# Performance work log

Hardware: AMD Instinct MI355X
Metric: run time of the kernel (lower is better)

## Reference

```python
import jax, jax.numpy as jnp
import numpy as np

DT = 1.0
S = 64            # num_sites
D = 2 * S         # state_dim
LOG_2PI = float(np.log(2.0 * np.pi))

def _selectors():
    s0 = np.zeros((2, 4), np.float32); s0[:, 0:2] = np.eye(2)
    s1 = np.zeros((2, 4), np.float32); s1[:, 2:4] = np.eye(2)
    cr = 0.5 * (s0 + s1)
    # [target=2, source=2, 2, 4]; off-diagonal pairs use the averaged selector
    return jnp.asarray(np.stack([np.stack([s0, cr]), np.stack([cr, s1])]))

SEL = _selectors()

def project_lon_lat(lon, lat):
    # lon, lat: [B,S]
    lat0 = lat.mean(-1, keepdims=True)
    lon0 = lon.mean(-1, keepdims=True)
    km = 111.32
    x = (lon - lon0) * (km * jnp.cos(jnp.deg2rad(lat0)))
    y = (lat - lat0) * km
    coords = jnp.stack([x, y], -1)                        # [B,S,2]
    h = coords[:, :, None, :] - coords[:, None, :, :]
    dist = jnp.sqrt((h ** 2).sum(-1) + 1e-12)
    npos = (dist > 1e-6).sum((-1, -2)).astype(coords.dtype)
    scale = dist.sum((-1, -2)) / jnp.maximum(npos, 1.0)
    return coords / jnp.maximum(scale, 1e-6)[:, None, None]

def build_A(h, mu, sigma, coupling, damping, eyeD):
    # h: [B,S,S,2], mu: [B,4], sigma: [B,4,4]
    B = mu.shape[0]
    sigma = 0.5 * (sigma + jnp.swapaxes(sigma, -1, -2))
    dm = jnp.einsum('tsab,nb->tsna', SEL, mu)                     # [2,2,B,2]
    dc = jnp.einsum('tsab,nbc,tsdc->tsnad', SEL, sigma, SEL)      # [2,2,B,2,2]
    dc = 0.5 * (dc + jnp.swapaxes(dc, -1, -2))
    eye2 = jnp.eye(2, dtype=h.dtype)
    Dm = (1.0 + 1e-4) * eye2 + (2.0 * DT ** 2) * dc
    Dinv = jnp.linalg.inv(Dm)
    _, logdet = jnp.linalg.slogdet(Dm)
    diff = h[None, None] - DT * dm[:, :, :, None, None, :]        # [2,2,B,S,S,2]
    q = jnp.einsum('tsbijd,tsbdf,tsbijf->tsbij', diff, Dinv, diff)
    ker = jnp.exp(-0.5 * (q + logdet[..., None, None]))
    ker = ker / jnp.maximum(ker.sum(-1, keepdims=True), 1e-6)
    ker = jnp.moveaxis(ker, 2, 0)                                 # [B,2,2,S,S]
    op = ker * coupling[None, :, :, None, None]
    op = jnp.transpose(op, (0, 1, 3, 2, 4)).reshape(B, D, D)
    return eyeD + DT * (op - damping * eyeD)

def _update(m, P, z_t, r2, eyeD):
    # Kalman measurement update with H = I, R = r2*I; returns per-sample NLL term
    Sm = P + r2 * eyeD
    v = z_t - m
    Sinv_v = jnp.linalg.solve(Sm, v[..., None])[..., 0]
    _, logdet = jnp.linalg.slogdet(Sm)
    nll_t = 0.5 * ((v * Sinv_v).sum(-1) + logdet + D * LOG_2PI)
    K = jnp.swapaxes(jnp.linalg.solve(Sm, P), -1, -2)   # P @ Sm^{-1} (P, Sm symmetric)
    m = m + jnp.einsum('bij,bj->bi', K, v)
    P = jnp.einsum('bij,bjk->bik', eyeD - K, P)
    return m, P, nll_t

def reference(z_seq, site_lon, site_lat, mu_seq, sigma_seq,
              log_q_proc, log_r_obs, log_p0, log_damping,
              init_mean, coupling_raw):
    B, T = z_seq.shape[0], z_seq.shape[1]
    z = z_seq.reshape(B, T, D)
    dtype = z.dtype
    eyeD = jnp.eye(D, dtype=dtype)
    r2 = jnp.exp(log_r_obs) ** 2
    q2 = jnp.exp(log_q_proc) ** 2
    damping = jnp.exp(log_damping)
    coupling = jnp.eye(2, dtype=dtype) + 0.25 * jnp.tanh(coupling_raw)

    lon = jnp.broadcast_to(site_lon[None], (B, S))
    lat = jnp.broadcast_to(site_lat[None], (B, S))
    coords = project_lon_lat(lon, lat)
    h = coords[:, :, None, :] - coords[:, None, :, :]   # [B,S,S,2]

    m0 = jnp.broadcast_to(init_mean[None], (B, D))
    P0 = jnp.broadcast_to(jnp.exp(log_p0) ** 2 * eyeD, (B, D, D))
    m, P, nll0 = _update(m0, P0, z[:, 0], r2, eyeD)

    def step(carry, xs):
        m, P = carry
        mu_t, sigma_t, z_t = xs
        A = build_A(h, mu_t, sigma_t, coupling, damping, eyeD)
        m = jnp.einsum('bij,bj->bi', A, m)
        P = jnp.einsum('bij,bjk,blk->bil', A, P, A) + q2 * eyeD
        m, P, nll_t = _update(m, P, z_t, r2, eyeD)
        return (m, P), nll_t

    xs = (jnp.swapaxes(mu_seq, 0, 1), jnp.swapaxes(sigma_seq, 0, 1),
          jnp.swapaxes(z[:, 1:], 0, 1))
    (_, _), nll_rest = jax.lax.scan(step, (m, P), xs)
    nll = nll0 + nll_rest.sum(0)   # [B]
    return nll.mean()

def setup_inputs() -> dict:
    key = jax.random.key(0)
    ks = jax.random.split(key, 5)
    B, T = 16, 128
    z_seq = jax.random.normal(ks[0], (B, T, S, 2), jnp.float32)
    site_lon = 10.0 + 0.5 * jax.random.uniform(ks[1], (S,), jnp.float32)
    site_lat = 55.0 + 0.5 * jax.random.uniform(ks[2], (S,), jnp.float32)
    mu_seq = 0.5 * jax.random.normal(ks[3], (B, T - 1, 4), jnp.float32)
    L = 0.2 * jax.random.normal(ks[4], (B, T - 1, 4, 4), jnp.float32)
    sigma_seq = jnp.einsum('btij,btkj->btik', L, L)   # PSD covariances
    return {
        'z_seq': z_seq, 'site_lon': site_lon, 'site_lat': site_lat,
        'mu_seq': mu_seq, 'sigma_seq': sigma_seq,
        'log_q_proc': jnp.float32(-2.0), 'log_r_obs': jnp.float32(-2.0),
        'log_p0': jnp.float32(0.0), 'log_damping': jnp.float32(0.0),
        'init_mean': jnp.zeros((D,), jnp.float32),
        'coupling_raw': jnp.zeros((2, 2), jnp.float32),
    }
```

## Files before the change

### kernel.cpp

```cpp
#include <hip/hip_runtime.h>
#include <math.h>


#define SQ 64
#define DQ 128
#define TQ 128
#define BQ 16
#define LDP 132
#define LDB 136
#define WFLOATS 17408
#define NTH 1024
#define LOG2PI 1.8378770664093454f

#define SMEM_FLOATS 35472

typedef __attribute__((ext_vector_type(8))) short bf16x8;
typedef __attribute__((ext_vector_type(4))) float f32x4;

__device__ __forceinline__ void lds_fence() {
  __asm__ volatile("s_waitcnt lgkmcnt(0)" ::: "memory");
}

__device__ __forceinline__ unsigned short f2bf(float f) {
  unsigned u = __float_as_uint(f);
  u += 0x7fffu + ((u >> 16) & 1u);
  return (unsigned short)(u >> 16);
}
__device__ __forceinline__ uint4 pack8(const float* v) {
  uint4 r;
  r.x = (unsigned)f2bf(v[0]) | ((unsigned)f2bf(v[1]) << 16);
  r.y = (unsigned)f2bf(v[2]) | ((unsigned)f2bf(v[3]) << 16);
  r.z = (unsigned)f2bf(v[4]) | ((unsigned)f2bf(v[5]) << 16);
  r.w = (unsigned)f2bf(v[6]) | ((unsigned)f2bf(v[7]) << 16);
  return r;
}

__device__ __forceinline__ float block_reduce_sum(float v, float* red) {
  #pragma unroll
  for (int off = 32; off > 0; off >>= 1) v += __shfl_down(v, off);
  const int tid = threadIdx.x;
  if ((tid & 63) == 0) red[tid >> 6] = v;
  __syncthreads();
  v = 0.0f;
  #pragma unroll
  for (int w = 0; w < NTH / 64; w++) v += red[w];
  __syncthreads();
  return v;
}

__device__ __forceinline__ void chol16_f(float* __restrict__ Wf,
                                         float* __restrict__ mdiag,
                                         int b0, int lane) {
  float a[16];
  if (lane < 16) {
    const float4* rp = (const float4*)(Wf + (b0 + lane) * LDP + b0);
    float4 q0 = rp[0], q1 = rp[1], q2v = rp[2], q3 = rp[3];
    a[0]=q0.x; a[1]=q0.y; a[2]=q0.z; a[3]=q0.w;
    a[4]=q1.x; a[5]=q1.y; a[6]=q1.z; a[7]=q1.w;
    a[8]=q2v.x; a[9]=q2v.y; a[10]=q2v.z; a[11]=q2v.w;
    a[12]=q3.x; a[13]=q3.y; a[14]=q3.z; a[15]=q3.w;
  } else {
    #pragma unroll
    for (int i = 0; i < 16; i++) a[i] = 1.0f;
  }
  float myrinv = 1.0f;
  #pragma unroll
  for (int j = 0; j < 16; j++) {
    float dj = __shfl(a[j], j);
    float rinv = rsqrtf(dj);
    float lij = a[j] * rinv;
    a[j] = lij;
    if (lane == j) myrinv = rinv;
    #pragma unroll
    for (int k = j + 1; k < 16; k++) {
      float lkj = __shfl(lij, k);
      a[k] = fmaf(-lij, lkj, a[k]);
    }
  }
  if (lane < 16) {
    float4* rp = (float4*)(Wf + (b0 + lane) * LDP + b0);
    rp[0] = make_float4(a[0], a[1], a[2], a[3]);
    rp[1] = make_float4(a[4], a[5], a[6], a[7]);
    rp[2] = make_float4(a[8], a[9], a[10], a[11]);
    rp[3] = make_float4(a[12], a[13], a[14], a[15]);
    mdiag[b0 + lane] = myrinv;
  }
}

__device__ __forceinline__ void trinv_chain2(float* __restrict__ Wf,
                                             const float* __restrict__ mdiag,
                                             int J, int pass, int lane) {
  const int c16 = lane & 15;
  const int j16 = 4 * (lane >> 4) + pass;
  const int sh = lane & 48;
  {
    float row[16];
    const float4* rp = (const float4*)(Wf + (J * 16 + c16) * LDP + J * 16);
    float4 a0 = rp[0], a1 = rp[1], a2 = rp[2], a3 = rp[3];
    row[0]=a0.x; row[1]=a0.y; row[2]=a0.z; row[3]=a0.w;
    row[4]=a1.x; row[5]=a1.y; row[6]=a1.z; row[7]=a1.w;
    row[8]=a2.x; row[9]=a2.y; row[10]=a2.z; row[11]=a2.w;
    row[12]=a3.x; row[13]=a3.y; row[14]=a3.z; row[15]=a3.w;
    float s = (c16 == j16) ? 1.0f : 0.0f;
    #pragma unroll
    for (int k = 0; k < 16; k++) {
      if (c16 == k) s *= mdiag[J * 16 + k];
      float sk = __shfl(s, sh | k);
      if (c16 > k) s = fmaf(-row[k], sk, s);
    }
    if (c16 > j16) Wf[(J * 16 + j16) * LDP + (J * 16 + c16)] = s;
  }
  lds_fence();
  const float md = mdiag[J * 16 + j16];
  const float* Mrow = Wf + (J * 16 + j16) * LDP + J * 16;
  #pragma unroll 1
  for (int I = J + 1; I < 8; I++) {
    const float* Lrow = Wf + (I * 16 + c16) * LDP + J * 16;
    float g = 0.0f;
    #pragma unroll
    for (int c4 = 0; c4 < 4; c4++) {
      float4 lv = *(const float4*)&Lrow[c4 * 4];
      float4 mq = *(const float4*)&Mrow[c4 * 4];
      float w0 = (c4*4+0 > j16) ? mq.x : ((c4*4+0 == j16) ? md : 0.0f);
      float w1 = (c4*4+1 > j16) ? mq.y : ((c4*4+1 == j16) ? md : 0.0f);
      float w2 = (c4*4+2 > j16) ? mq.z : ((c4*4+2 == j16) ? md : 0.0f);
      float w3 = (c4*4+3 > j16) ? mq.w : ((c4*4+3 == j16) ? md : 0.0f);
      g = fmaf(lv.x, w0, g); g = fmaf(lv.y, w1, g);
      g = fmaf(lv.z, w2, g); g = fmaf(lv.w, w3, g);
    }
    for (int K = J + 1; K < I; K++) {
      const float* LK = Lrow + (K - J) * 16;
      const float* MK = Wf + (J * 16 + j16) * LDP + K * 16;
      #pragma unroll
      for (int c4 = 0; c4 < 4; c4++) {
        float4 lv = *(const float4*)&LK[c4 * 4];
        float4 mq = *(const float4*)&MK[c4 * 4];
        g = fmaf(lv.x, mq.x, g); g = fmaf(lv.y, mq.y, g);
        g = fmaf(lv.z, mq.z, g); g = fmaf(lv.w, mq.w, g);
      }
    }
    float row2[16];
    {
      const float4* rp2 = (const float4*)(Wf + (I * 16 + c16) * LDP + I * 16);
      float4 a0 = rp2[0], a1 = rp2[1], a2 = rp2[2], a3 = rp2[3];
      row2[0]=a0.x; row2[1]=a0.y; row2[2]=a0.z; row2[3]=a0.w;
      row2[4]=a1.x; row2[5]=a1.y; row2[6]=a1.z; row2[7]=a1.w;
      row2[8]=a2.x; row2[9]=a2.y; row2[10]=a2.z; row2[11]=a2.w;
      row2[12]=a3.x; row2[13]=a3.y; row2[14]=a3.z; row2[15]=a3.w;
    }
    float sv = g;
    #pragma unroll
    for (int k = 0; k < 16; k++) {
      if (c16 == k) sv *= mdiag[I * 16 + k];
      float sk = __shfl(sv, sh | k);
      if (c16 > k) sv = fmaf(-row2[k], sk, sv);
    }
    Wf[(J * 16 + j16) * LDP + (I * 16 + c16)] = -sv;
    lds_fence();
  }
}

extern "C" __global__ __launch_bounds__(NTH, 4)
void ide_kf_kernel(const float* __restrict__ z_seq,
                   const float* __restrict__ site_lon,
                   const float* __restrict__ site_lat,
                   const float* __restrict__ mu_seq,
                   const float* __restrict__ sigma_seq,
                   const float* __restrict__ log_q,
                   const float* __restrict__ log_r,
                   const float* __restrict__ log_p0,
                   const float* __restrict__ log_damp,
                   const float* __restrict__ init_mean,
                   const float* __restrict__ coupling_raw,
                   float* __restrict__ ws) {
  extern __shared__ float smem[];
  float* Wf     = smem;
  float* B1f    = Wf + WFLOATS;
  float* B2f    = B1f + 8704;
  float* coords = B2f + 8704;
  float* mv     = coords + 128;
  float* vv     = mv + DQ;
  float* yv     = vv + DQ;
  float* mdiag  = yv + DQ;
  float* red    = mdiag + DQ;

  unsigned short* Tb  = (unsigned short*)Wf;
  unsigned short* Ab  = (unsigned short*)B1f;
  unsigned short* Mtb = (unsigned short*)B1f;
  unsigned short* Pb  = (unsigned short*)B2f;

  const int tid = threadIdx.x;
  const int lane = tid & 63;
  const int wave = tid >> 6;
  const int rb = wave >> 1, ch = wave & 1;
  const int m16 = lane & 15, quad = lane >> 4;
  const int grp = wave >> 2, pass = wave & 3;
  const int b = blockIdx.x;
  float* nll_out = ws;

  const float r2 = __expf(2.0f * log_r[0]);
  const float q2 = __expf(2.0f * log_q[0]);
  const float p0sq = __expf(2.0f * log_p0[0]);
  const float damping = __expf(log_damp[0]);
  const float cpl00 = 1.0f + 0.25f * tanhf(coupling_raw[0]);
  const float cpl01 = 0.25f * tanhf(coupling_raw[1]);
  const float cpl10 = 0.25f * tanhf(coupling_raw[2]);
  const float cpl11 = 1.0f + 0.25f * tanhf(coupling_raw[3]);

  float myLon = (tid < SQ) ? site_lon[tid] : 0.0f;
  float myLat = (tid < SQ) ? site_lat[tid] : 0.0f;
  float lat0 = block_reduce_sum(myLat, red) * (1.0f / 64.0f);
  float lon0 = block_reduce_sum(myLon, red) * (1.0f / 64.0f);
  if (tid < SQ) {
    const float km = 111.32f;
    float cs = cosf(lat0 * 0.017453292519943295f);
    coords[2 * tid]     = (myLon - lon0) * (km * cs);
    coords[2 * tid + 1] = (myLat - lat0) * km;
  }
  __syncthreads();
  float dsum = 0.0f, dcnt = 0.0f;
  for (int idx = tid; idx < SQ * SQ; idx += NTH) {
    int i = idx >> 6, j = idx & 63;
    float dx = coords[2 * i] - coords[2 * j];
    float dy = coords[2 * i + 1] - coords[2 * j + 1];
    float d = sqrtf(dx * dx + dy * dy + 1e-12f);
    dsum += d;
    if (d > 1e-6f) dcnt += 1.0f;
  }
  dsum = block_reduce_sum(dsum, red);
  dcnt = block_reduce_sum(dcnt, red);
  float scale = dsum / fmaxf(dcnt, 1.0f);
  float sdiv = 1.0f / fmaxf(scale, 1e-6f);
  if (tid < SQ) { coords[2 * tid] *= sdiv; coords[2 * tid + 1] *= sdiv; }

  for (int e = tid; e < WFLOATS / 4; e += NTH)
    ((float4*)Wf)[e] = make_float4(0.0f, 0.0f, 0.0f, 0.0f);
  for (int e = tid; e < 8704 / 4; e += NTH)
    ((float4*)B2f)[e] = make_float4(0.0f, 0.0f, 0.0f, 0.0f);
  __syncthreads();
  if (tid < DQ) {
    Wf[tid * LDP + tid] = p0sq + r2;
    Pb[tid * LDB + tid] = f2bf(p0sq);
    mv[tid] = init_mean[tid];
  }
  __syncthreads();

  float nllp = 0.0f;

  #pragma unroll 1
  for (int t = 0; t < TQ; t++) {
    const float* zt = z_seq + ((size_t)b * TQ + t) * DQ;

    if (t > 0) {
      const float* mu_t = mu_seq + ((size_t)b * (TQ - 1) + (t - 1)) * 4;
      const float* sg_t = sigma_seq + ((size_t)b * (TQ - 1) + (t - 1)) * 16;

      {
        const int unit = tid >> 2, q = tid & 3;
        const int r = unit >> 1, ss = unit & 1, tt = r >> 6, i = r & 63;
        float m0 = mu_t[0], m1 = mu_t[1], m2 = mu_t[2], m3 = mu_t[3];
        float dmx, dmy, c00, c01, c11;
        if (tt == 0 && ss == 0) {
          dmx = m0; dmy = m1;
          c00 = sg_t[0]; c01 = 0.5f * (sg_t[1] + sg_t[4]); c11 = sg_t[5];
        } else if (tt == 1 && ss == 1) {
          dmx = m2; dmy = m3;
          c00 = sg_t[10]; c01 = 0.5f * (sg_t[11] + sg_t[14]); c11 = sg_t[15];
        } else {
          dmx = 0.5f * (m0 + m2); dmy = 0.5f * (m1 + m3);
          float s00 = sg_t[0];
          float s02 = 0.5f * (sg_t[2] + sg_t[8]);
          float s22 = sg_t[10];
          float s01 = 0.5f * (sg_t[1] + sg_t[4]);
          float s03 = 0.5f * (sg_t[3] + sg_t[12]);
          float s21 = 0.5f * (sg_t[9] + sg_t[6]);
          float s23 = 0.5f * (sg_t[11] + sg_t[14]);
          float s11 = sg_t[5];
          float s13 = 0.5f * (sg_t[7] + sg_t[13]);
          float s33 = sg_t[15];
          c00 = 0.25f * (s00 + s02 + s02 + s22);
          c01 = 0.25f * (s01 + s03 + s21 + s23);
          c11 = 0.25f * (s11 + s13 + s13 + s33);
        }
        float D00 = 1.0001f + 2.0f * c00;
        float D01 = 2.0f * c01;
        float D11 = 1.0001f + 2.0f * c11;
        float det = D00 * D11 - D01 * D01;
        float dinv = 1.0f / det;
        float d00 = D11 * dinv, d01 = -D01 * dinv, d11 = D00 * dinv;
        float ldts = __logf(det);
        float cix = coords[2 * i], ciy = coords[2 * i + 1];
        const float* cj = coords + q * 32;
        float kv[16];
        float rsum = 0.0f;
        #pragma unroll
        for (int u = 0; u < 16; u++) {
          float dx = cix - cj[2 * u] - dmx;
          float dy = ciy - cj[2 * u + 1] - dmy;
          float qf = d00 * dx * dx + 2.0f * d01 * dx * dy + d11 * dy * dy;
          kv[u] = __expf(-0.5f * (qf + ldts));
          rsum += kv[u];
        }
        float rtot = rsum + __shfl_xor(rsum, 1);
        rtot += __shfl_xor(rtot, 2);
        float cv = (tt == 0) ? ((ss == 0) ? cpl00 : cpl01)
                             : ((ss == 0) ? cpl10 : cpl11);
        float norm = cv / fmaxf(rtot, 1e-6f);
        #pragma unroll
        for (int u = 0; u < 16; u++) kv[u] *= norm;
        if (ss == tt && ((i >> 4) == q)) kv[i & 15] += 1.0f - damping;
        unsigned short* arow = Ab + r * LDB + ss * 64 + q * 16;
        *(uint4*)(arow) = pack8(kv);
        *(uint4*)(arow + 8) = pack8(kv + 8);
      }
      __syncthreads();

      {
        f32x4 acc[4];
        #pragma unroll
        for (int c = 0; c < 4; c++) acc[c] = (f32x4){0.0f, 0.0f, 0.0f, 0.0f};
        #pragma unroll
        for (int ks = 0; ks < 4; ks++) {
          const int ko = 32 * ks + 8 * quad;
          bf16x8 a = *(const bf16x8*)(Ab + (16 * rb + m16) * LDB + ko);
          #pragma unroll
          for (int ct = 0; ct < 4; ct++) {
            bf16x8 bb = *(const bf16x8*)(Pb + (64 * ch + 16 * ct + m16) * LDB + ko);
            acc[ct] = __builtin_amdgcn_mfma_f32_16x16x32_bf16(a, bb, acc[ct], 0, 0, 0);
          }
        }
        #pragma unroll
        for (int ct = 0; ct < 4; ct++)
          #pragma unroll
          for (int reg = 0; reg < 4; reg++)
            Tb[(16 * rb + 4 * quad + reg) * LDB + 64 * ch + 16 * ct + m16] =
                f2bf(acc[ct][reg]);
        __syncthreads();
      }

      {
        const int ctmax = rb - 4 * ch;
        f32x4 acc[4];
        #pragma unroll
        for (int c = 0; c < 4; c++) acc[c] = (f32x4){0.0f, 0.0f, 0.0f, 0.0f};
        const bool gemv_wave = (wave == 1 || wave == 3);
        const int grow = (wave == 1) ? lane : 64 + lane;
        float newm = 0.0f;
        if (ctmax >= 0) {
          #pragma unroll
          for (int ks = 0; ks < 4; ks++) {
            const int ko = 32 * ks + 8 * quad;
            bf16x8 a = *(const bf16x8*)(Tb + (16 * rb + m16) * LDB + ko);
            #pragma unroll
            for (int ct = 0; ct < 4; ct++) {
              if (ct <= ctmax) {
                bf16x8 bb = *(const bf16x8*)(Ab + (64 * ch + 16 * ct + m16) * LDB + ko);
                acc[ct] = __builtin_amdgcn_mfma_f32_16x16x32_bf16(a, bb, acc[ct], 0, 0, 0);
              }
            }
          }
        } else if (gemv_wave) {
          const unsigned* ar = (const unsigned*)(Ab + grow * LDB);
          #pragma unroll 8
          for (int k2 = 0; k2 < 64; k2++) {
            unsigned p = ar[k2];
            newm = fmaf(__uint_as_float(p << 16), mv[2 * k2], newm);
            newm = fmaf(__uint_as_float(p & 0xffff0000u), mv[2 * k2 + 1], newm);
          }
        }
        __syncthreads();
        if (ctmax >= 0) {
          #pragma unroll
          for (int ct = 0; ct < 4; ct++) {
            if (ct <= ctmax) {
              #pragma unroll
              for (int reg = 0; reg < 4; reg++) {
                const int rg = 16 * rb + 4 * quad + reg;
                const int cgl = 64 * ch + 16 * ct + m16;
                Wf[rg * LDP + cgl] = acc[ct][reg] + ((rg == cgl) ? (q2 + r2) : 0.0f);
              }
            }
          }
        }
        if (gemv_wave) vv[grow] = zt[grow] - newm;
        if (wave == 0) {
          lds_fence();
          chol16_f(Wf, mdiag, 0, lane);
        }
        __syncthreads();
      }
    }

    if (t == 0) {
      if (tid < 64) {
        chol16_f(Wf, mdiag, 0, lane);
      } else if (tid < 192) {
        const int i = tid - 64;
        vv[i] = zt[i] - mv[i];
      }
      __syncthreads();
    }

    #pragma unroll 1
    for (int kb = 0; kb < 7; kb++) {
      const int b0k = kb * 16, base = b0k + 16, nbelow = DQ - base;
      if (tid < nbelow) {
        const int r = base + tid;
        float* wr = Wf + r * LDP + b0k;
        float w[16];
        #pragma unroll
        for (int u4 = 0; u4 < 4; u4++) {
          float4 w4 = *(const float4*)&wr[u4 * 4];
          w[u4*4] = w4.x; w[u4*4+1] = w4.y; w[u4*4+2] = w4.z; w[u4*4+3] = w4.w;
        }
        #pragma unroll
        for (int j = 0; j < 16; j++) {
          float s = w[j];
          #pragma unroll
          for (int l = 0; l < 16; l++) {
            if (l < j) s = fmaf(-w[l], Wf[(b0k + j) * LDP + b0k + l], s);
          }
          w[j] = s * mdiag[b0k + j];
        }
        #pragma unroll
        for (int u4 = 0; u4 < 4; u4++)
          *(float4*)&wr[u4 * 4] =
              make_float4(w[u4*4], w[u4*4+1], w[u4*4+2], w[u4*4+3]);
      }
      __syncthreads();
      if (tid < 64) {
        #pragma unroll
        for (int u = 0; u < 4; u++) {
          const int o = lane * 4 + u;
          const int mr = o >> 4, mc = o & 15;
          if (mr >= mc) {
            const float* pi = Wf + (base + mr) * LDP + b0k;
            const float* pj = Wf + (base + mc) * LDP + b0k;
            float s = 0.0f;
            #pragma unroll
            for (int c4 = 0; c4 < 4; c4++) {
              float4 xa = *(const float4*)&pi[c4 * 4];
              float4 yb = *(const float4*)&pj[c4 * 4];
              s = fmaf(xa.x, yb.x, s); s = fmaf(xa.y, yb.y, s);
              s = fmaf(xa.z, yb.z, s); s = fmaf(xa.w, yb.w, s);
            }
            Wf[(base + mr) * LDP + base + mc] -= s;
          }
        }
        chol16_f(Wf, mdiag, base, lane);
      } else if (tid >= 256) {
        const int grq = (tid >> 8) - 1;
        const int t8 = tid & 255;
        const int mrow = t8 >> 4, mcol = t8 & 15;
        const int mb = 7 - kb;
        int cnt = 0;
        for (int bi = 0; bi < mb; bi++) {
          for (int bj = 0; bj <= bi; bj++) {
            if (bi | bj) {
              if (cnt % 3 == grq && (bi > bj || mrow >= mcol)) {
                const int i = base + bi * 16 + mrow;
                const int j = base + bj * 16 + mcol;
                const float* pi = Wf + i * LDP + b0k;
                const float* pj = Wf + j * LDP + b0k;
                float s = 0.0f;
                #pragma unroll
                for (int c4 = 0; c4 < 4; c4++) {
                  float4 xa = *(const float4*)&pi[c4 * 4];
                  float4 yb = *(const float4*)&pj[c4 * 4];
                  s = fmaf(xa.x, yb.x, s); s = fmaf(xa.y, yb.y, s);
                  s = fmaf(xa.z, yb.z, s); s = fmaf(xa.w, yb.w, s);
                }
                Wf[i * LDP + j] -= s;
              }
              cnt++;
            }
          }
        }
      }
      __syncthreads();
    }

    {
      #pragma unroll 1
      for (int cc = 0; cc < 2; cc++) {
        const int J = cc ? (7 - grp) : grp;
        trinv_chain2(Wf, mdiag, J, pass, lane);
      }
      __syncthreads();
    }

    {
      const int mrow = tid >> 3, kc = (tid & 7) * 16;
      float mtv[16];
      if (kc > mrow) {
        const float4* rp = (const float4*)(Wf + mrow * LDP + kc);
        float4 q0 = rp[0], q1 = rp[1], q2v = rp[2], q3 = rp[3];
        mtv[0]=q0.x; mtv[1]=q0.y; mtv[2]=q0.z; mtv[3]=q0.w;
        mtv[4]=q1.x; mtv[5]=q1.y; mtv[6]=q1.z; mtv[7]=q1.w;
        mtv[8]=q2v.x; mtv[9]=q2v.y; mtv[10]=q2v.z; mtv[11]=q2v.w;
        mtv[12]=q3.x; mtv[13]=q3.y; mtv[14]=q3.z; mtv[15]=q3.w;
      } else if (kc + 15 < mrow) {
        #pragma unroll
        for (int u = 0; u < 16; u++) mtv[u] = 0.0f;
      } else {
        #pragma unroll
        for (int u = 0; u < 16; u++) {
          const int k = kc + u;
          mtv[u] = (k > mrow) ? Wf[mrow * LDP + k]
                 : ((k == mrow) ? mdiag[mrow] : 0.0f);
        }
      }
      if (tid < DQ) {
        nllp -= __logf(mdiag[tid]);
        float s = mdiag[tid] * vv[tid];
        for (int k = 0; k < tid; k++) s = fmaf(Wf[k * LDP + tid], vv[k], s);
        yv[tid] = s;
      }
      unsigned short* mt = Mtb + mrow * LDB + kc;
      *(uint4*)(mt) = pack8(mtv);
      *(uint4*)(mt + 8) = pack8(mtv + 8);
      __syncthreads();
    }

    {
      f32x4 acc[4];
      #pragma unroll
      for (int c = 0; c < 4; c++) acc[c] = (f32x4){0.0f, 0.0f, 0.0f, 0.0f};
      if (tid < DQ) nllp += 0.5f * yv[tid] * yv[tid];
      const int ctmax = rb - 4 * ch;
      if (ctmax >= 0) {
        for (int ks = (rb >> 1); ks < 4; ks++) {
          const int ko = 32 * ks + 8 * quad;
          bf16x8 a = *(const bf16x8*)(Mtb + (16 * rb + m16) * LDB + ko);
          #pragma unroll
          for (int ct = 0; ct < 4; ct++) {
            if (ct <= ctmax) {
              bf16x8 bb = *(const bf16x8*)(Mtb + (64 * ch + 16 * ct + m16) * LDB + ko);
              acc[ct] = __builtin_amdgcn_mfma_f32_16x16x32_bf16(a, bb, acc[ct], 0, 0, 0);
            }
          }
        }
      }
      const float nr22 = -r2 * r2;
      #pragma unroll
      for (int ct = 0; ct < 4; ct++) {
        if (ct <= ctmax) {
          const bool strict = (ct < ctmax);
          #pragma unroll
          for (int reg = 0; reg < 4; reg++) {
            const int rg = 16 * rb + 4 * quad + reg;
            const int cgl = 64 * ch + 16 * ct + m16;
            unsigned short hv = f2bf(nr22 * acc[ct][reg] + ((rg == cgl) ? r2 : 0.0f));
            Pb[rg * LDB + cgl] = hv;
            if (strict) Pb[cgl * LDB + rg] = hv;
          }
        }
      }
      if (tid < DQ) {
        const unsigned* mr = (const unsigned*)(Mtb + tid * LDB);
        float s = 0.0f;
        #pragma unroll 8
        for (int k2 = 0; k2 < 64; k2++) {
          unsigned p = mr[k2];
          s = fmaf(__uint_as_float(p << 16), yv[2 * k2], s);
          s = fmaf(__uint_as_float(p & 0xffff0000u), yv[2 * k2 + 1], s);
        }
        mv[tid] = zt[tid] - r2 * s;
      }
      __syncthreads();
    }
  }

  float total = block_reduce_sum(nllp, red);
  if (tid == 0)
    nll_out[b] = total + (float)TQ * 0.5f * (float)DQ * LOG2PI;
}

extern "C" __global__ void ide_finalize(const float* __restrict__ part,
                                        float* __restrict__ out) {
  if (threadIdx.x == 0) {
    float s = 0.0f;
    for (int i = 0; i < BQ; i++) s += part[i];
    out[0] = s * (1.0f / BQ);
  }
}

extern "C" void kernel_launch(void* const* d_in, const int* in_sizes, int n_in,
                              void* d_out, int out_size, void* d_ws, size_t ws_size,
                              hipStream_t stream) {
  (void)in_sizes; (void)n_in; (void)out_size; (void)ws_size;
  const float* z_seq        = (const float*)d_in[0];
  const float* site_lon     = (const float*)d_in[1];
  const float* site_lat     = (const float*)d_in[2];
  const float* mu_seq       = (const float*)d_in[3];
  const float* sigma_seq    = (const float*)d_in[4];
  const float* log_q        = (const float*)d_in[5];
  const float* log_r        = (const float*)d_in[6];
  const float* log_p0       = (const float*)d_in[7];
  const float* log_damp     = (const float*)d_in[8];
  const float* init_mean    = (const float*)d_in[9];
  const float* coupling_raw = (const float*)d_in[10];
  float* ws = (float*)d_ws;
  float* out = (float*)d_out;

  const size_t smem_bytes = (size_t)SMEM_FLOATS * sizeof(float);
  hipFuncSetAttribute((const void*)ide_kf_kernel,
                      hipFuncAttributeMaxDynamicSharedMemorySize,
                      (int)smem_bytes);

  hipLaunchKernelGGL(ide_kf_kernel, dim3(BQ), dim3(NTH), smem_bytes, stream,
                     z_seq, site_lon, site_lat, mu_seq, sigma_seq,
                     log_q, log_r, log_p0, log_damp, init_mean, coupling_raw,
                     ws);
  hipLaunchKernelGGL(ide_finalize, dim3(1), dim3(64), 0, stream, ws, out);
}
```

Before: 9.552 ms.

## Software-pipeline blocked Cholesky with lookahead on the next panel

Restructures the blocked Cholesky loop so each iteration cuts the barriers per block step from two to one. Wave 0 applies the previous block column's update to the next diagonal block, does its triangular solve and rank update, then factors that block. Waves 1-2 apply the deferred update and the triangular solve to the remaining rows. The trailing-update waves apply the previous block column's update, lagging one step behind. This removes one __syncthreads per block step on the serial critical path, at the cost of redundant recomputation in wave 0 and subtle ordering dependencies.

```diff
diff --git a/kernel.cpp b/kernel.cpp
--- a/kernel.cpp
+++ b/kernel.cpp
@@ -403,52 +403,148 @@
 
     #pragma unroll 1
     for (int kb = 0; kb < 7; kb++) {
-      const int b0k = kb * 16, base = b0k + 16, nbelow = DQ - base;
-      if (tid < nbelow) {
-        const int r = base + tid;
-        float* wr = Wf + r * LDP + b0k;
-        float w[16];
-        #pragma unroll
-        for (int u4 = 0; u4 < 4; u4++) {
-          float4 w4 = *(const float4*)&wr[u4 * 4];
-          w[u4*4] = w4.x; w[u4*4+1] = w4.y; w[u4*4+2] = w4.z; w[u4*4+3] = w4.w;
-        }
-        #pragma unroll
-        for (int j = 0; j < 16; j++) {
-          float s = w[j];
-          #pragma unroll
-          for (int l = 0; l < 16; l++) {
-            if (l < j) s = fmaf(-w[l], Wf[(b0k + j) * LDP + b0k + l], s);
-          }
-          w[j] = s * mdiag[b0k + j];
-        }
-        #pragma unroll
-        for (int u4 = 0; u4 < 4; u4++)
-          *(float4*)&wr[u4 * 4] =
-              make_float4(w[u4*4], w[u4*4+1], w[u4*4+2], w[u4*4+3]);
-      }
-      __syncthreads();
-      if (tid < 64) {
-        #pragma unroll
-        for (int u = 0; u < 4; u++) {
-          const int o = lane * 4 + u;
-          const int mr = o >> 4, mc = o & 15;
-          if (mr >= mc) {
-            const float* pi = Wf + (base + mr) * LDP + b0k;
-            const float* pj = Wf + (base + mc) * LDP + b0k;
+      const int b0k = kb * 16;
+      const int bm1 = b0k - 16;
+      const int nb1 = b0k + 16;
+      if (wave == 0) {
+        const int r16 = lane & 15, q4 = lane >> 4;
+        const int growr = nb1 + r16;
+        float w[16], lp[16];
+        {
+          const float4* rp = (const float4*)(Wf + growr * LDP + b0k);
+          float4 a0 = rp[0], a1 = rp[1], a2 = rp[2], a3 = rp[3];
+          w[0]=a0.x; w[1]=a0.y; w[2]=a0.z; w[3]=a0.w;
+          w[4]=a1.x; w[5]=a1.y; w[6]=a1.z; w[7]=a1.w;
+          w[8]=a2.x; w[9]=a2.y; w[10]=a2.z; w[11]=a2.w;
+          w[12]=a3.x; w[13]=a3.y; w[14]=a3.z; w[15]=a3.w;
+        }
+        if (kb > 0) {
+          const float4* rp = (const float4*)(Wf + growr * LDP + bm1);
+          float4 a0 = rp[0], a1 = rp[1], a2 = rp[2], a3 = rp[3];
+          lp[0]=a0.x; lp[1]=a0.y; lp[2]=a0.z; lp[3]=a0.w;
+          lp[4]=a1.x; lp[5]=a1.y; lp[6]=a1.z; lp[7]=a1.w;
+          lp[8]=a2.x; lp[9]=a2.y; lp[10]=a2.z; lp[11]=a2.w;
+          lp[12]=a3.x; lp[13]=a3.y; lp[14]=a3.z; lp[15]=a3.w;
+          #pragma unroll
+          for (int c = 0; c < 16; c++) {
+            const float* Lr = Wf + (b0k + c) * LDP + bm1;
             float s = 0.0f;
             #pragma unroll
             for (int c4 = 0; c4 < 4; c4++) {
-              float4 xa = *(const float4*)&pi[c4 * 4];
-              float4 yb = *(const float4*)&pj[c4 * 4];
-              s = fmaf(xa.x, yb.x, s); s = fmaf(xa.y, yb.y, s);
-              s = fmaf(xa.z, yb.z, s); s = fmaf(xa.w, yb.w, s);
-            }
-            Wf[(base + mr) * LDP + base + mc] -= s;
-          }
-        }
-        chol16_f(Wf, mdiag, base, lane);
-      } else if (tid >= 256) {
+              float4 lv = *(const float4*)&Lr[c4 * 4];
+              s = fmaf(lp[c4*4+0], lv.x, s);
+              s = fmaf(lp[c4*4+1], lv.y, s);
+              s = fmaf(lp[c4*4+2], lv.z, s);
+              s = fmaf(lp[c4*4+3], lv.w, s);
+            }
+            w[c] -= s;
+          }
+        } else {
+          #pragma unroll
+          for (int c = 0; c < 16; c++) lp[c] = 0.0f;
+        }
+        #pragma unroll
+        for (int j = 0; j < 16; j++) {
+          float s = w[j];
+          const float* Ld = Wf + (b0k + j) * LDP + b0k;
+          #pragma unroll
+          for (int l = 0; l < 16; l++) {
+            if (l < j) s = fmaf(-w[l], Ld[l], s);
+          }
+          w[j] = s * mdiag[b0k + j];
+        }
+        if (q4 == 0) {
+          float4* wp = (float4*)(Wf + growr * LDP + b0k);
+          wp[0] = make_float4(w[0], w[1], w[2], w[3]);
+          wp[1] = make_float4(w[4], w[5], w[6], w[7]);
+          wp[2] = make_float4(w[8], w[9], w[10], w[11]);
+          wp[3] = make_float4(w[12], w[13], w[14], w[15]);
+        }
+        lds_fence();
+        #pragma unroll
+        for (int cc = 0; cc < 4; cc++) {
+          const int c = q4 + 4 * cc;
+          if (c <= r16) {
+            const float* Lck = Wf + (nb1 + c) * LDP + b0k;
+            float s = 0.0f;
+            #pragma unroll
+            for (int c4 = 0; c4 < 4; c4++) {
+              float4 lv = *(const float4*)&Lck[c4 * 4];
+              s = fmaf(w[c4*4+0], lv.x, s);
+              s = fmaf(w[c4*4+1], lv.y, s);
+              s = fmaf(w[c4*4+2], lv.z, s);
+              s = fmaf(w[c4*4+3], lv.w, s);
+            }
+            if (kb > 0) {
+              const float* Lcm = Wf + (nb1 + c) * LDP + bm1;
+              #pragma unroll
+              for (int c4 = 0; c4 < 4; c4++) {
+                float4 lv = *(const float4*)&Lcm[c4 * 4];
+                s = fmaf(lp[c4*4+0], lv.x, s);
+                s = fmaf(lp[c4*4+1], lv.y, s);
+                s = fmaf(lp[c4*4+2], lv.z, s);
+                s = fmaf(lp[c4*4+3], lv.w, s);
+              }
+            }
+            Wf[(nb1 + r16) * LDP + (nb1 + c)] -= s;
+          }
+        }
+        lds_fence();
+        chol16_f(Wf, mdiag, nb1, lane);
+      } else if (wave <= 2) {
+        const int rr = tid - 64;
+        const int nrows = 96 - 16 * kb;
+        if (rr < nrows) {
+          const int r = (kb + 2) * 16 + rr;
+          float w[16];
+          {
+            const float4* rp = (const float4*)(Wf + r * LDP + b0k);
+            float4 a0 = rp[0], a1 = rp[1], a2 = rp[2], a3 = rp[3];
+            w[0]=a0.x; w[1]=a0.y; w[2]=a0.z; w[3]=a0.w;
+            w[4]=a1.x; w[5]=a1.y; w[6]=a1.z; w[7]=a1.w;
+            w[8]=a2.x; w[9]=a2.y; w[10]=a2.z; w[11]=a2.w;
+            w[12]=a3.x; w[13]=a3.y; w[14]=a3.z; w[15]=a3.w;
+          }
+          if (kb > 0) {
+            float lp[16];
+            const float4* rp = (const float4*)(Wf + r * LDP + bm1);
+            float4 a0 = rp[0], a1 = rp[1], a2 = rp[2], a3 = rp[3];
+            lp[0]=a0.x; lp[1]=a0.y; lp[2]=a0.z; lp[3]=a0.w;
+            lp[4]=a1.x; lp[5]=a1.y; lp[6]=a1.z; lp[7]=a1.w;
+            lp[8]=a2.x; lp[9]=a2.y; lp[10]=a2.z; lp[11]=a2.w;
+            lp[12]=a3.x; lp[13]=a3.y; lp[14]=a3.z; lp[15]=a3.w;
+            #pragma unroll
+            for (int c = 0; c < 16; c++) {
+              const float* Lr = Wf + (b0k + c) * LDP + bm1;
+              float s = 0.0f;
+              #pragma unroll
+              for (int c4 = 0; c4 < 4; c4++) {
+                float4 lv = *(const float4*)&Lr[c4 * 4];
+                s = fmaf(lp[c4*4+0], lv.x, s);
+                s = fmaf(lp[c4*4+1], lv.y, s);
+                s = fmaf(lp[c4*4+2], lv.z, s);
+                s = fmaf(lp[c4*4+3], lv.w, s);
+              }
+              w[c] -= s;
+            }
+          }
+          #pragma unroll
+          for (int j = 0; j < 16; j++) {
+            float s = w[j];
+            const float* Ld = Wf + (b0k + j) * LDP + b0k;
+            #pragma unroll
+            for (int l = 0; l < 16; l++) {
+              if (l < j) s = fmaf(-w[l], Ld[l], s);
+            }
+            w[j] = s * mdiag[b0k + j];
+          }
+          float4* wp = (float4*)(Wf + r * LDP + b0k);
+          wp[0] = make_float4(w[0], w[1], w[2], w[3]);
+          wp[1] = make_float4(w[4], w[5], w[6], w[7]);
+          wp[2] = make_float4(w[8], w[9], w[10], w[11]);
+          wp[3] = make_float4(w[12], w[13], w[14], w[15]);
+        }
+      } else if (tid >= 256 && kb > 0) {
         const int grq = (tid >> 8) - 1;
         const int t8 = tid & 255;
         const int mrow = t8 >> 4, mcol = t8 & 15;
@@ -458,10 +554,10 @@
           for (int bj = 0; bj <= bi; bj++) {
             if (bi | bj) {
               if (cnt % 3 == grq && (bi > bj || mrow >= mcol)) {
-                const int i = base + bi * 16 + mrow;
-                const int j = base + bj * 16 + mcol;
-                const float* pi = Wf + i * LDP + b0k;
-                const float* pj = Wf + j * LDP + b0k;
+                const int i = nb1 + bi * 16 + mrow;
+                const int j = nb1 + bj * 16 + mcol;
+                const float* pi = Wf + i * LDP + bm1;
+                const float* pj = Wf + j * LDP + bm1;
                 float s = 0.0f;
                 #pragma unroll
                 for (int c4 = 0; c4 < 4; c4++) {
```

Result: slower. 10.83 ms (+13.3%).
